# Kernel tuning notes

Measured on AMD Instinct MI355X. Metric: run time of the kernel, lower is better.

The kernel has to match this reference:

```python
import jax, jax.numpy as jnp
import numpy as np

N, E, T, F, HID, NCLS = 50000, 800000, 6, 64, 48, 2
LN_EPS = 1e-5


def setup_inputs() -> dict:
    key = jax.random.key(0)
    ks = jax.random.split(key, 24)
    p = lambda k, shape, s=0.1: jax.random.normal(k, shape, dtype=jnp.float32) * s
    inp = {
        "x_seq": jax.random.normal(ks[0], (T, N, F), dtype=jnp.float32),
        "edge_index": jax.random.randint(ks[1], (2, E), 0, N, dtype=jnp.int64),
        "edge_weight": jax.random.uniform(ks[2], (E,), dtype=jnp.float32),
        # GCN layer 0
        "W0": p(ks[3], (F, HID)), "b0": jnp.zeros((HID,), jnp.float32),
        "g0": jnp.ones((HID,), jnp.float32), "be0": jnp.zeros((HID,), jnp.float32),
        # GCN layer 1
        "W1": p(ks[4], (HID, HID)), "b1": jnp.zeros((HID,), jnp.float32),
        "g1": jnp.ones((HID,), jnp.float32), "be1": jnp.zeros((HID,), jnp.float32),
        # GRU (torch gate order: r, z, n)
        "W_ih": p(ks[5], (3 * HID, HID)), "W_hh": p(ks[6], (3 * HID, HID)),
        "b_ih": jnp.zeros((3 * HID,), jnp.float32), "b_hh": jnp.zeros((3 * HID,), jnp.float32),
        # classifier MLP
        "Wc1": p(ks[7], (HID, HID // 2)), "bc1": jnp.zeros((HID // 2,), jnp.float32),
        "Wc2": p(ks[8], (HID // 2, NCLS)), "bc2": jnp.zeros((NCLS,), jnp.float32),
    }
    return inp


def _layer_norm(x, g, b):
    mu = x.mean(-1, keepdims=True)
    var = ((x - mu) ** 2).mean(-1, keepdims=True)
    return (x - mu) * jax.lax.rsqrt(var + LN_EPS) * g + b


def reference(x_seq, edge_index, edge_weight, W0, b0, g0, be0, W1, b1, g1, be1,
              W_ih, W_hh, b_ih, b_hh, Wc1, bc1, Wc2, bc2):
    n = x_seq.shape[1]
    hid = W0.shape[1]
    row, col = edge_index[0], edge_index[1]
    # PyG GCNConv default: add self-loops (weight 1), symmetric normalization
    loop = jnp.arange(n)
    row_f = jnp.concatenate([row, loop])
    col_f = jnp.concatenate([col, loop])
    w_f = jnp.concatenate([edge_weight, jnp.ones((n,), edge_weight.dtype)])
    deg = jax.ops.segment_sum(w_f, col_f, num_segments=n)
    dis = jnp.where(deg > 0, jax.lax.rsqrt(jnp.maximum(deg, 1e-12)), 0.0)
    norm = dis[row_f] * w_f * dis[col_f]  # [E+N]

    def gcn(x, W, b):
        h = x @ W                              # [N, hid]
        msg = h[row_f] * norm[:, None]         # [E+N, hid]
        return jax.ops.segment_sum(msg, col_f, num_segments=n) + b

    def spatial(x_t):
        # layer 0: no residual (in_dim != hid)
        h1 = jax.nn.relu(_layer_norm(gcn(x_t, W0, b0), g0, be0))
        # layer 1: residual (dropout is eval-mode no-op)
        h2 = jax.nn.relu(_layer_norm(gcn(h1, W1, b1), g1, be1)) + h1
        return h2

    # sequential map over T keeps per-step [E,hid] message buffers small
    H = jax.lax.map(spatial, x_seq)            # [T, N, hid]

    def gru_step(h, x_t):
        gi = x_t @ W_ih.T + b_ih               # [N, 3*hid]
        gh = h @ W_hh.T + b_hh
        i_r, i_z, i_n = jnp.split(gi, 3, axis=-1)
        h_r, h_z, h_n = jnp.split(gh, 3, axis=-1)
        r = jax.nn.sigmoid(i_r + h_r)
        z = jax.nn.sigmoid(i_z + h_z)
        nv = jnp.tanh(i_n + r * h_n)
        h_new = (1.0 - z) * nv + z * h
        return h_new, None

    h0 = jnp.zeros((n, hid), x_seq.dtype)
    z_last, _ = jax.lax.scan(gru_step, h0, H)  # last hidden state [N, hid]

    logits = jax.nn.relu(z_last @ Wc1 + bc1) @ Wc2 + bc2  # [N, 2]
    return logits
```

## Files before the change

kernel.cpp:

```cpp
#include <hip/hip_runtime.h>
#include <math.h>

#define NN 50000
#define NE 800000
#define TT 6
#define HID 48
#define NB 196
#define LR 65

__device__ __forceinline__ float sigmoidf_(float x){ return 1.0f/(1.0f+__expf(-x)); }
__device__ __forceinline__ float tanhf_(float x){
  float xc = fminf(fmaxf(x,-15.f),15.f);
  float t = __expf(2.f*xc);
  return (t-1.f)/(t+1.f);
}
__device__ __forceinline__ unsigned f2bf(float x){
  unsigned u = __float_as_uint(x);
  return (u + 0x7fffu + ((u>>16)&1u)) >> 16;
}
__device__ __forceinline__ unsigned pack2(float a, float b){
  return f2bf(a) | (f2bf(b)<<16);
}
__device__ __forceinline__ float bflo(unsigned u){ return __uint_as_float(u<<16); }
__device__ __forceinline__ float bfhi(unsigned u){ return __uint_as_float(u & 0xffff0000u); }

struct U3 { unsigned x,y,z; };

__device__ __forceinline__ int block_scan_incl(int x, int* wsum){
  int lane = threadIdx.x & 63, w = threadIdx.x >> 6;
  int v = x;
#pragma unroll
  for(int d=1; d<64; d<<=1){
    int u = __shfl_up(v, d, 64);
    if(lane >= d) v += u;
  }
  if(lane==63) wsum[w] = v;
  __syncthreads();
  int add = 0;
#pragma unroll
  for(int k=0;k<3;k++) if(w>k) add += wsum[k];
  return v + add;
}

__global__ __launch_bounds__(256) void k_setup(int* cnt,
                                               const float* __restrict__ Wih, const float* __restrict__ Whh,
                                               float* Wg){
  int i = blockIdx.x*256+threadIdx.x;
  if(i<NN) cnt[i]=0;
  if(i < 6*48*48){
    int w = i/2304, rem = i%2304;
    int k = rem/48, g8 = rem%48;
    int g = g8>>3, j = g8&7;
    int col = w*8+j;
    float v = (g<3) ? Wih[(g*48+col)*48 + k] : Whh[((g-3)*48+col)*48 + k];
    Wg[i] = v;
  }
}

__global__ __launch_bounds__(256) void k_cnt(const int* __restrict__ ei, int* cnt, int* pos){
  int e = blockIdx.x*256+threadIdx.x;
  if(e<NE){
    int c = ei[NE+e];
    pos[e] = atomicAdd(&cnt[c], 1);
  }
}

__global__ __launch_bounds__(256) void k_partA(const int* __restrict__ cnt, int* bsum){
  __shared__ int wsum[4];
  int i = blockIdx.x*256+threadIdx.x;
  int x = (i<NN)? cnt[i] : 0;
  int lane = threadIdx.x & 63, w = threadIdx.x >> 6;
  int v = x;
#pragma unroll
  for(int m=32;m>=1;m>>=1) v += __shfl_xor(v, m, 64);
  if(lane==0) wsum[w]=v;
  __syncthreads();
  if(threadIdx.x==0) bsum[blockIdx.x] = wsum[0]+wsum[1]+wsum[2]+wsum[3];
}

__global__ __launch_bounds__(256) void k_midB(const int* __restrict__ bsum, int* bpre, int* offs){
  __shared__ int wsum[4];
  int t = threadIdx.x;
  int x = (t<NB)? bsum[t] : 0;
  int incl = block_scan_incl(x, wsum);
  if(t<NB) bpre[t] = incl - x;
  if(t==255) offs[NN] = incl;
}

__global__ __launch_bounds__(256) void k_offsC(const int* __restrict__ cnt, const int* __restrict__ bpre,
                                               int* offs){
  __shared__ int wsum[4];
  int i = blockIdx.x*256+threadIdx.x;
  int x = (i<NN)? cnt[i] : 0;
  int incl = block_scan_incl(x, wsum);
  if(i<NN) offs[i] = bpre[blockIdx.x] + incl - x;
}

__global__ __launch_bounds__(256) void k_scatter(const int* __restrict__ ei, const float* __restrict__ ew,
                                                 const int* __restrict__ offs, const int* __restrict__ pos,
                                                 int2* __restrict__ csr){
  int e = blockIdx.x*256+threadIdx.x;
  if(e<NE){
    int c = ei[NE+e];
    int2 v; v.x = ei[e]; v.y = __float_as_int(ew[e]);
    csr[offs[c]+pos[e]] = v;
  }
}

__global__ __launch_bounds__(256) void k_deg(const int2* __restrict__ csr, const int* __restrict__ offs,
                                             float* dis){
  int i = blockIdx.x*256+threadIdx.x;
  if(i<NN){
    float s = 1.f;
    int e0=offs[i], e1=offs[i+1];
    for(int j=e0;j<e1;j++) s += __int_as_float(csr[j].y);
    dis[i] = rsqrtf(s);
  }
}

__global__ __launch_bounds__(256) void k_normE(int2* __restrict__ csr, const float* __restrict__ dis){
  int j = blockIdx.x*256+threadIdx.x;
  if(j<NE){
    int2 v = csr[j];
    v.y = __float_as_int(dis[v.x]*__int_as_float(v.y));
    csr[j] = v;
  }
}

__global__ __launch_bounds__(256) void k_mm0(const float* __restrict__ X, const float* __restrict__ W,
                                             unsigned* __restrict__ A){
  int s = __builtin_amdgcn_readfirstlane(threadIdx.x>>6);
  int n = blockIdx.x*64 + (threadIdx.x&63);
  if(n>=NN) return;
  const float* xb = X + (long long)n*64;
  const float* wb = W + 12*s;
  float acc[TT][12];
#pragma unroll
  for(int t=0;t<TT;t++)
#pragma unroll
    for(int j=0;j<12;j++) acc[t][j]=0.f;
#pragma unroll 2
  for(int k4=0;k4<16;k4++){
    float4 xv[TT];
#pragma unroll
    for(int t=0;t<TT;t++) xv[t] = *reinterpret_cast<const float4*>(xb + (long long)t*NN*64 + 4*k4);
#pragma unroll
    for(int q=0;q<4;q++){
      const float* wr = wb + (4*k4+q)*HID;
      float w[12];
#pragma unroll
      for(int j=0;j<12;j++) w[j]=wr[j];
#pragma unroll
      for(int t=0;t<TT;t++){
        float xs = (&xv[t].x)[q];
#pragma unroll
        for(int j=0;j<12;j++) acc[t][j] = fmaf(xs, w[j], acc[t][j]);
      }
    }
  }
  unsigned buf[36];
#pragma unroll
  for(int j=0;j<12;j++){
    buf[3*j  ]=pack2(acc[0][j],acc[1][j]);
    buf[3*j+1]=pack2(acc[2][j],acc[3][j]);
    buf[3*j+2]=pack2(acc[4][j],acc[5][j]);
  }
  uint4* o4 = reinterpret_cast<uint4*>(A + (long long)n*144 + 36*s);
#pragma unroll
  for(int q=0;q<9;q++) o4[q] = make_uint4(buf[4*q],buf[4*q+1],buf[4*q+2],buf[4*q+3]);
}

__global__ __launch_bounds__(256) void k_mm1(const float* __restrict__ X, const float* __restrict__ W,
                                             unsigned* __restrict__ A){
  int s = __builtin_amdgcn_readfirstlane(threadIdx.x>>6);
  int n = blockIdx.x*64 + (threadIdx.x&63);
  if(n>=NN) return;
  const float* xb = X + (long long)n*(TT*HID);
  const float* wb = W + 12*s;
  float acc[TT][12];
#pragma unroll
  for(int t=0;t<TT;t++)
#pragma unroll
    for(int j=0;j<12;j++) acc[t][j]=0.f;
#pragma unroll 2
  for(int k4=0;k4<12;k4++){
    float4 xv[TT];
#pragma unroll
    for(int t=0;t<TT;t++) xv[t] = *reinterpret_cast<const float4*>(xb + t*HID + 4*k4);
#pragma unroll
    for(int q=0;q<4;q++){
      const float* wr = wb + (4*k4+q)*HID;
      float w[12];
#pragma unroll
      for(int j=0;j<12;j++) w[j]=wr[j];
#pragma unroll
      for(int t=0;t<TT;t++){
        float xs = (&xv[t].x)[q];
#pragma unroll
        for(int j=0;j<12;j++) acc[t][j] = fmaf(xs, w[j], acc[t][j]);
      }
    }
  }
  unsigned buf[36];
#pragma unroll
  for(int j=0;j<12;j++){
    buf[3*j  ]=pack2(acc[0][j],acc[1][j]);
    buf[3*j+1]=pack2(acc[2][j],acc[3][j]);
    buf[3*j+2]=pack2(acc[4][j],acc[5][j]);
  }
  uint4* o4 = reinterpret_cast<uint4*>(A + (long long)n*144 + 36*s);
#pragma unroll
  for(int q=0;q<9;q++) o4[q] = make_uint4(buf[4*q],buf[4*q+1],buf[4*q+2],buf[4*q+3]);
}

__global__ __launch_bounds__(256) void k_agg(const unsigned* __restrict__ A, const float* __restrict__ bias,
                                             const float* __restrict__ gain, const float* __restrict__ beta,
                                             const float* __restrict__ resid, float* __restrict__ out,
                                             const int* __restrict__ offs, const int2* __restrict__ csr,
                                             const float* __restrict__ dis){
  int wid = (blockIdx.x*256+threadIdx.x)>>6;
  int lane = threadIdx.x & 63;
  if(wid>=NN) return;
  const bool act = lane<HID;
  const int f = act? lane : (HID-1);
  float dn = dis[wid];
  float acc[TT];
  {
    U3 v = *reinterpret_cast<const U3*>(A + (long long)wid*144 + 3*f);
    acc[0]=dn*bflo(v.x); acc[1]=dn*bfhi(v.x);
    acc[2]=dn*bflo(v.y); acc[3]=dn*bfhi(v.y);
    acc[4]=dn*bflo(v.z); acc[5]=dn*bfhi(v.z);
  }
  int e0=offs[wid], e1=offs[wid+1];
  int e=e0;
  for(; e+3<e1; e+=4){
    int2 i0=csr[e], i1=csr[e+1], i2=csr[e+2], i3=csr[e+3];
    U3 d0 = *reinterpret_cast<const U3*>(A + (long long)i0.x*144 + 3*f);
    U3 d1 = *reinterpret_cast<const U3*>(A + (long long)i1.x*144 + 3*f);
    U3 d2 = *reinterpret_cast<const U3*>(A + (long long)i2.x*144 + 3*f);
    U3 d3 = *reinterpret_cast<const U3*>(A + (long long)i3.x*144 + 3*f);
    float n0=__int_as_float(i0.y), n1=__int_as_float(i1.y);
    float n2=__int_as_float(i2.y), n3=__int_as_float(i3.y);
    acc[0]=fmaf(n0,bflo(d0.x),acc[0]); acc[1]=fmaf(n0,bfhi(d0.x),acc[1]);
    acc[2]=fmaf(n0,bflo(d0.y),acc[2]); acc[3]=fmaf(n0,bfhi(d0.y),acc[3]);
    acc[4]=fmaf(n0,bflo(d0.z),acc[4]); acc[5]=fmaf(n0,bfhi(d0.z),acc[5]);
    acc[0]=fmaf(n1,bflo(d1.x),acc[0]); acc[1]=fmaf(n1,bfhi(d1.x),acc[1]);
    acc[2]=fmaf(n1,bflo(d1.y),acc[2]); acc[3]=fmaf(n1,bfhi(d1.y),acc[3]);
    acc[4]=fmaf(n1,bflo(d1.z),acc[4]); acc[5]=fmaf(n1,bfhi(d1.z),acc[5]);
    acc[0]=fmaf(n2,bflo(d2.x),acc[0]); acc[1]=fmaf(n2,bfhi(d2.x),acc[1]);
    acc[2]=fmaf(n2,bflo(d2.y),acc[2]); acc[3]=fmaf(n2,bfhi(d2.y),acc[3]);
    acc[4]=fmaf(n2,bflo(d2.z),acc[4]); acc[5]=fmaf(n2,bfhi(d2.z),acc[5]);
    acc[0]=fmaf(n3,bflo(d3.x),acc[0]); acc[1]=fmaf(n3,bfhi(d3.x),acc[1]);
    acc[2]=fmaf(n3,bflo(d3.y),acc[2]); acc[3]=fmaf(n3,bfhi(d3.y),acc[3]);
    acc[4]=fmaf(n3,bflo(d3.z),acc[4]); acc[5]=fmaf(n3,bfhi(d3.z),acc[5]);
  }
  for(; e<e1; ++e){
    int2 i0=csr[e];
    U3 d0 = *reinterpret_cast<const U3*>(A + (long long)i0.x*144 + 3*f);
    float n0=__int_as_float(i0.y);
    acc[0]=fmaf(n0,bflo(d0.x),acc[0]); acc[1]=fmaf(n0,bfhi(d0.x),acc[1]);
    acc[2]=fmaf(n0,bflo(d0.y),acc[2]); acc[3]=fmaf(n0,bfhi(d0.y),acc[3]);
    acc[4]=fmaf(n0,bflo(d0.z),acc[4]); acc[5]=fmaf(n0,bfhi(d0.z),acc[5]);
  }
  float bb = bias[f], gg = gain[f], be = beta[f];
  const float rn = 1.0f/HID;
#pragma unroll
  for(int t=0;t<TT;t++){
    float val = fmaf(acc[t], dn, bb);
    float v = act? val : 0.f;
    float s = v, s2 = v*v;
#pragma unroll
    for(int m=32;m>=1;m>>=1){
      s  += __shfl_xor(s,  m, 64);
      s2 += __shfl_xor(s2, m, 64);
    }
    float mu  = s*rn;
    float var = fmaxf(s2*rn - mu*mu, 0.f);
    float y = (val-mu)*rsqrtf(var+1e-5f)*gg + be;
    y = fmaxf(y, 0.f);
    long long oidx = (long long)wid*(TT*HID) + t*HID + f;
    if(resid) y += resid[oidx];
    if(act) out[oidx] = y;
  }
}

__global__ __launch_bounds__(384) void k_gruF(const float* __restrict__ X,
                                              const float* __restrict__ Wg,
                                              const float* __restrict__ bih, const float* __restrict__ bhh,
                                              const float* __restrict__ Wc1, const float* __restrict__ bc1,
                                              const float* __restrict__ Wc2, const float* __restrict__ bc2,
                                              float* __restrict__ out){
  __shared__ float xbuf[48*LR];
  __shared__ float hbuf[48*LR];
  int tid = threadIdx.x;
  int wv = __builtin_amdgcn_readfirstlane(tid>>6);
  int lane = tid & 63;
  int f0 = wv*8;
  long long nbase = (long long)blockIdx.x*64;

  for(int i=tid;i<48*LR;i+=384) hbuf[i]=0.f;

  float rb[8], zb[8], nbi[8], nbh[8];
#pragma unroll
  for(int j=0;j<8;j++){
    int f=f0+j;
    rb[j]  = bih[f]    + bhh[f];
    zb[j]  = bih[48+f] + bhh[48+f];
    nbi[j] = bih[96+f];
    nbh[j] = bhh[96+f];
  }

  for(int t=0;t<TT;t++){
#pragma unroll
    for(int i=0;i<2;i++){
      int c = tid + 384*i;
      int nd = c/12, fc = c - nd*12;
      long long gn = nbase + nd; if(gn>NN-1) gn=NN-1;
      float4 xv = *reinterpret_cast<const float4*>(X + gn*(TT*HID) + t*HID + fc*4);
      int base = (fc*4)*LR + nd;
      xbuf[base]      = xv.x;
      xbuf[base+LR]   = xv.y;
      xbuf[base+2*LR] = xv.z;
      xbuf[base+3*LR] = xv.w;
    }
    __syncthreads();

    float ra[8],za[8],ia[8],ha[8];
#pragma unroll
    for(int j=0;j<8;j++){ ra[j]=za[j]=ia[j]=ha[j]=0.f; }

#pragma unroll 2
    for(int k=0;k<48;k++){
      const float* wp = Wg + ((wv*48 + k)*48);
      float ws[48];
#pragma unroll
      for(int q=0;q<48;q++) ws[q]=wp[q];
      float xk = xbuf[k*LR+lane];
      float hk = hbuf[k*LR+lane];
#pragma unroll
      for(int j=0;j<8;j++){
        ra[j]=fmaf(xk,ws[j],   ra[j]); ra[j]=fmaf(hk,ws[24+j],ra[j]);
        za[j]=fmaf(xk,ws[8+j], za[j]); za[j]=fmaf(hk,ws[32+j],za[j]);
        ia[j]=fmaf(xk,ws[16+j],ia[j]); ha[j]=fmaf(hk,ws[40+j],ha[j]);
      }
    }

    float hn[8];
#pragma unroll
    for(int j=0;j<8;j++){
      float r  = sigmoidf_(ra[j]+rb[j]);
      float zg = sigmoidf_(za[j]+zb[j]);
      float ng = tanhf_(ia[j]+nbi[j] + r*(ha[j]+nbh[j]));
      hn[j] = (1.f-zg)*ng + zg*hbuf[(f0+j)*LR+lane];
    }
    __syncthreads();
#pragma unroll
    for(int j=0;j<8;j++) hbuf[(f0+j)*LR+lane] = hn[j];
  }
  __syncthreads();

  if(wv==0){
    long long gn = nbase + lane;
    if(gn<NN){
      float hv[24];
#pragma unroll
      for(int j=0;j<24;j++) hv[j]=bc1[j];
      for(int k=0;k<HID;k++){
        float xk = hbuf[k*LR+lane];
        const float* wr = Wc1 + k*24;
#pragma unroll
        for(int j=0;j<24;j++) hv[j] = fmaf(xk, wr[j], hv[j]);
      }
      float l0=bc2[0], l1=bc2[1];
#pragma unroll
      for(int j=0;j<24;j++){
        float a = fmaxf(hv[j],0.f);
        l0 = fmaf(a, Wc2[2*j],   l0);
        l1 = fmaf(a, Wc2[2*j+1], l1);
      }
      reinterpret_cast<float2*>(out)[gn] = make_float2(l0,l1);
    }
  }
}

static inline size_t al256(size_t x){ return (x+255)&~(size_t)255; }

extern "C" void kernel_launch(void* const* d_in, const int* in_sizes, int n_in,
                              void* d_out, int out_size, void* d_ws, size_t ws_size,
                              hipStream_t stream){
  const float* x_seq=(const float*)d_in[0];
  const int*   ei   =(const int*)d_in[1];
  const float* ew   =(const float*)d_in[2];
  const float* W0=(const float*)d_in[3];  const float* b0=(const float*)d_in[4];
  const float* g0=(const float*)d_in[5];  const float* be0=(const float*)d_in[6];
  const float* W1=(const float*)d_in[7];  const float* b1=(const float*)d_in[8];
  const float* g1=(const float*)d_in[9];  const float* be1=(const float*)d_in[10];
  const float* Wih=(const float*)d_in[11];const float* Whh=(const float*)d_in[12];
  const float* bih=(const float*)d_in[13];const float* bhh=(const float*)d_in[14];
  const float* Wc1=(const float*)d_in[15];const float* bc1=(const float*)d_in[16];
  const float* Wc2=(const float*)d_in[17];const float* bc2=(const float*)d_in[18];
  float* outp=(float*)d_out;

  char* p=(char*)d_ws; size_t off=0;
  auto alloc=[&](size_t bytes)->void*{ void* r=p+off; off=al256(off+bytes); return r; };
  float* dis    =(float*)alloc((size_t)NN*4);
  int*   cnt    =(int*)  alloc((size_t)NN*4);
  int*   offs   =(int*)  alloc((size_t)(NN+1)*4);
  int*   bsum   =(int*)  alloc((size_t)NB*4);
  int*   bpre   =(int*)  alloc((size_t)NB*4);
  int*   pos    =(int*)  alloc((size_t)NE*4);
  int2*  csr    =(int2*) alloc((size_t)NE*8);
  float* Wg     =(float*)alloc((size_t)6*48*48*4);
  unsigned* A   =(unsigned*)alloc((size_t)NN*576 + 1024);
  float* h1     =(float*)alloc((size_t)NN*TT*HID*4);
  float* h2     =(float*)alloc((size_t)NN*TT*HID*4);

  const int GN=(NN+255)/256, GE=(NE+255)/256;
  const int GMM=(NN+63)/64;
  const int GAGG=(NN*64+255)/256;
  const int GGRU=(NN+63)/64;

  k_setup  <<<GN,256,0,stream>>>(cnt,Wih,Whh,Wg);
  k_cnt    <<<GE,256,0,stream>>>(ei,cnt,pos);
  k_partA  <<<NB,256,0,stream>>>(cnt,bsum);
  k_midB   <<<1,256,0,stream>>>(bsum,bpre,offs);
  k_offsC  <<<NB,256,0,stream>>>(cnt,bpre,offs);
  k_scatter<<<GE,256,0,stream>>>(ei,ew,offs,pos,csr);
  k_deg    <<<GN,256,0,stream>>>(csr,offs,dis);
  k_normE  <<<GE,256,0,stream>>>(csr,dis);

  k_mm0<<<GMM,256,0,stream>>>(x_seq, W0, A);
  k_agg<<<GAGG,256,0,stream>>>(A,b0,g0,be0,nullptr,h1,offs,csr,dis);
  k_mm1<<<GMM,256,0,stream>>>(h1, W1, A);
  k_agg<<<GAGG,256,0,stream>>>(A,b1,g1,be1,h1,h2,offs,csr,dis);
  k_gruF<<<GGRU,384,0,stream>>>(h2, Wg, bih,bhh, Wc1,bc1,Wc2,bc2, outp);
}
```

Before: 705.6 us.

## Hoist GRU input projection into a separate batched kernel with bf16 storage

Result: slower. 727.8 us (+3.1%).

```diff
diff --git a/kernel.cpp b/kernel.cpp
--- a/kernel.cpp
+++ b/kernel.cpp
@@ -8,6 +8,8 @@
 #define NB 196
 #define LR 65
 
+typedef unsigned short ushortT;
+
 __device__ __forceinline__ float sigmoidf_(float x){ return 1.0f/(1.0f+__expf(-x)); }
 __device__ __forceinline__ float tanhf_(float x){
   float xc = fminf(fmaxf(x,-15.f),15.f);
@@ -23,6 +25,7 @@
 }
 __device__ __forceinline__ float bflo(unsigned u){ return __uint_as_float(u<<16); }
 __device__ __forceinline__ float bfhi(unsigned u){ return __uint_as_float(u & 0xffff0000u); }
+__device__ __forceinline__ float bfu(ushortT u){ return __uint_as_float(((unsigned)u)<<16); }
 
 struct U3 { unsigned x,y,z; };
 
@@ -44,16 +47,19 @@
 
 __global__ __launch_bounds__(256) void k_setup(int* cnt,
                                                const float* __restrict__ Wih, const float* __restrict__ Whh,
-                                               float* Wg){
+                                               float* Wp, float* Wgh){
   int i = blockIdx.x*256+threadIdx.x;
   if(i<NN) cnt[i]=0;
-  if(i < 6*48*48){
-    int w = i/2304, rem = i%2304;
-    int k = rem/48, g8 = rem%48;
-    int g = g8>>3, j = g8&7;
-    int col = w*8+j;
-    float v = (g<3) ? Wih[(g*48+col)*48 + k] : Whh[((g-3)*48+col)*48 + k];
-    Wg[i] = v;
+  if(i < 6912){
+    int g = i/2304, rem = i%2304;
+    int k = rem/48, f = rem%48;
+    Wp[i] = Wih[(g*48+f)*48 + k];
+  } else if(i < 13824){
+    int idx = i-6912;
+    int wv = idx/1152, rem = idx%1152;
+    int k = rem/24, m = rem%24;
+    int g = m>>3, j = m&7;
+    Wgh[idx] = Whh[(g*48+wv*8+j)*48 + k];
   }
 }
 
@@ -284,13 +290,42 @@
   }
 }
 
-__global__ __launch_bounds__(384) void k_gruF(const float* __restrict__ X,
-                                              const float* __restrict__ Wg,
-                                              const float* __restrict__ bih, const float* __restrict__ bhh,
+__global__ __launch_bounds__(256) void k_mmG(const float* __restrict__ h2, const float* __restrict__ Wp,
+                                             const float* __restrict__ bih, ushortT* __restrict__ gi){
+  int g = blockIdx.x, t = blockIdx.y;
+  int n = blockIdx.z*256 + threadIdx.x;
+  if(n>=NN) return;
+  const float* xr = h2 + (size_t)n*(TT*HID) + t*HID;
+  const float* wb = Wp + g*2304;
+  const float* bb = bih + g*48;
+  float acc[48];
+#pragma unroll
+  for(int j=0;j<48;j++) acc[j]=bb[j];
+#pragma unroll 2
+  for(int k4=0;k4<12;k4++){
+    float4 xv = *reinterpret_cast<const float4*>(xr + 4*k4);
+#pragma unroll
+    for(int q=0;q<4;q++){
+      const float* wr = wb + (4*k4+q)*48;
+      float w[48];
+#pragma unroll
+      for(int j=0;j<48;j++) w[j]=wr[j];
+      float xs = (&xv.x)[q];
+#pragma unroll
+      for(int j=0;j<48;j++) acc[j] = fmaf(xs, w[j], acc[j]);
+    }
+  }
+  size_t base = ((size_t)t*144 + g*48)*NN + n;
+#pragma unroll
+  for(int j=0;j<48;j++) gi[base + (size_t)j*NN] = (ushortT)f2bf(acc[j]);
+}
+
+__global__ __launch_bounds__(384) void k_gruF(const ushortT* __restrict__ gi,
+                                              const float* __restrict__ Wgh,
+                                              const float* __restrict__ bhh,
                                               const float* __restrict__ Wc1, const float* __restrict__ bc1,
                                               const float* __restrict__ Wc2, const float* __restrict__ bc2,
                                               float* __restrict__ out){
-  __shared__ float xbuf[48*LR];
   __shared__ float hbuf[48*LR];
   int tid = threadIdx.x;
   int wv = __builtin_amdgcn_readfirstlane(tid>>6);
@@ -300,57 +335,53 @@
 
   for(int i=tid;i<48*LR;i+=384) hbuf[i]=0.f;
 
-  float rb[8], zb[8], nbi[8], nbh[8];
+  float bhr[8], bhz[8], bhn[8];
 #pragma unroll
   for(int j=0;j<8;j++){
     int f=f0+j;
-    rb[j]  = bih[f]    + bhh[f];
-    zb[j]  = bih[48+f] + bhh[48+f];
-    nbi[j] = bih[96+f];
-    nbh[j] = bhh[96+f];
+    bhr[j] = bhh[f];
+    bhz[j] = bhh[48+f];
+    bhn[j] = bhh[96+f];
   }
 
   for(int t=0;t<TT;t++){
-#pragma unroll
-    for(int i=0;i<2;i++){
-      int c = tid + 384*i;
-      int nd = c/12, fc = c - nd*12;
-      long long gn = nbase + nd; if(gn>NN-1) gn=NN-1;
-      float4 xv = *reinterpret_cast<const float4*>(X + gn*(TT*HID) + t*HID + fc*4);
-      int base = (fc*4)*LR + nd;
-      xbuf[base]      = xv.x;
-      xbuf[base+LR]   = xv.y;
-      xbuf[base+2*LR] = xv.z;
-      xbuf[base+3*LR] = xv.w;
+    float gr[8], gz[8], gn_[8];
+    {
+      const ushortT* gp = gi + ((size_t)t*144 + f0)*NN + nbase + lane;
+#pragma unroll
+      for(int j=0;j<8;j++){
+        gr[j]  = bfu(gp[(size_t)j*NN]);
+        gz[j]  = bfu(gp[(size_t)(48+j)*NN]);
+        gn_[j] = bfu(gp[(size_t)(96+j)*NN]);
+      }
     }
     __syncthreads();
 
-    float ra[8],za[8],ia[8],ha[8];
-#pragma unroll
-    for(int j=0;j<8;j++){ ra[j]=za[j]=ia[j]=ha[j]=0.f; }
-
-#pragma unroll 2
+    float ar[8],az[8],an[8];
+#pragma unroll
+    for(int j=0;j<8;j++){ ar[j]=az[j]=an[j]=0.f; }
+
+#pragma unroll 4
     for(int k=0;k<48;k++){
-      const float* wp = Wg + ((wv*48 + k)*48);
-      float ws[48];
-#pragma unroll
-      for(int q=0;q<48;q++) ws[q]=wp[q];
-      float xk = xbuf[k*LR+lane];
+      const float* wp = Wgh + (wv*48 + k)*24;
+      float ws[24];
+#pragma unroll
+      for(int q=0;q<24;q++) ws[q]=wp[q];
       float hk = hbuf[k*LR+lane];
 #pragma unroll
       for(int j=0;j<8;j++){
-        ra[j]=fmaf(xk,ws[j],   ra[j]); ra[j]=fmaf(hk,ws[24+j],ra[j]);
-        za[j]=fmaf(xk,ws[8+j], za[j]); za[j]=fmaf(hk,ws[32+j],za[j]);
-        ia[j]=fmaf(xk,ws[16+j],ia[j]); ha[j]=fmaf(hk,ws[40+j],ha[j]);
+        ar[j]=fmaf(hk,ws[j],   ar[j]);
+        az[j]=fmaf(hk,ws[8+j], az[j]);
+        an[j]=fmaf(hk,ws[16+j],an[j]);
       }
     }
 
     float hn[8];
 #pragma unroll
     for(int j=0;j<8;j++){
-      float r  = sigmoidf_(ra[j]+rb[j]);
-      float zg = sigmoidf_(za[j]+zb[j]);
-      float ng = tanhf_(ia[j]+nbi[j] + r*(ha[j]+nbh[j]));
+      float r  = sigmoidf_(gr[j] + ar[j] + bhr[j]);
+      float zg = sigmoidf_(gz[j] + az[j] + bhz[j]);
+      float ng = tanhf_(gn_[j] + r*(an[j] + bhn[j]));
       hn[j] = (1.f-zg)*ng + zg*hbuf[(f0+j)*LR+lane];
     }
     __syncthreads();
@@ -410,17 +441,19 @@
   int*   bpre   =(int*)  alloc((size_t)NB*4);
   int*   pos    =(int*)  alloc((size_t)NE*4);
   int2*  csr    =(int2*) alloc((size_t)NE*8);
-  float* Wg     =(float*)alloc((size_t)6*48*48*4);
+  float* Wp     =(float*)alloc((size_t)3*48*48*4);
+  float* Wgh    =(float*)alloc((size_t)6*48*24*4);
   unsigned* A   =(unsigned*)alloc((size_t)NN*576 + 1024);
   float* h1     =(float*)alloc((size_t)NN*TT*HID*4);
   float* h2     =(float*)alloc((size_t)NN*TT*HID*4);
+  ushortT* gi   =(ushortT*)A;
 
   const int GN=(NN+255)/256, GE=(NE+255)/256;
   const int GMM=(NN+63)/64;
   const int GAGG=(NN*64+255)/256;
   const int GGRU=(NN+63)/64;
 
-  k_setup  <<<GN,256,0,stream>>>(cnt,Wih,Whh,Wg);
+  k_setup  <<<GN,256,0,stream>>>(cnt,Wih,Whh,Wp,Wgh);
   k_cnt    <<<GE,256,0,stream>>>(ei,cnt,pos);
   k_partA  <<<NB,256,0,stream>>>(cnt,bsum);
   k_midB   <<<1,256,0,stream>>>(bsum,bpre,offs);
@@ -433,5 +466,6 @@
   k_agg<<<GAGG,256,0,stream>>>(A,b0,g0,be0,nullptr,h1,offs,csr,dis);
   k_mm1<<<GMM,256,0,stream>>>(h1, W1, A);
   k_agg<<<GAGG,256,0,stream>>>(A,b1,g1,be1,h1,h2,offs,csr,dis);
-  k_gruF<<<GGRU,384,0,stream>>>(h2, Wg, bih,bhh, Wc1,bc1,Wc2,bc2, outp);
-}
+  k_mmG<<<dim3(3,6,NB),256,0,stream>>>(h2, Wp, bih, gi);
+  k_gruF<<<GGRU,384,0,stream>>>(gi, Wgh, bhh, Wc1,bc1,Wc2,bc2, outp);
+}
```
